# Performance work log

Hardware: AMD Instinct MI355X
Metric: run time of the kernel (lower is better)

## Reference

```python
import jax, jax.numpy as jnp
import numpy as np
from jax import lax

NEG = -1e30


def ctc_loss(log_probs, targets, input_lengths, target_lengths, blank=0):
    """CTC loss per sample (reduction='none').
    log_probs: [B,T,C] log-softmaxed. targets: [B,S] int (values != blank).
    Returns [B] negative log likelihoods.
    """
    B, T, C = log_probs.shape
    S = targets.shape[1]
    L = 2 * S + 1
    # extended label sequence with blanks interleaved: [b, t1, b, t2, ..., b]
    blanks = jnp.full((B, S), blank, targets.dtype)
    ext = jnp.concatenate(
        [jnp.stack([blanks, targets], axis=-1).reshape(B, 2 * S),
         jnp.full((B, 1), blank, targets.dtype)], axis=1)  # [B,L]
    # skip-transition allowed where ext[l] != blank and ext[l] != ext[l-2]
    prev2 = jnp.concatenate([jnp.full((B, 2), -1, ext.dtype), ext[:, :-2]], axis=1)
    allow_skip = (ext != blank) & (ext != prev2)  # [B,L]

    lp0 = jnp.take_along_axis(log_probs[:, 0, :], ext, axis=1)  # [B,L]
    alpha0 = jnp.where(jnp.arange(L)[None, :] < 2, lp0, NEG)

    def step(alpha, lp_t):  # lp_t: [B,C]
        lp = jnp.take_along_axis(lp_t, ext, axis=1)  # [B,L]
        a1 = alpha
        a2 = jnp.concatenate([jnp.full((B, 1), NEG), alpha[:, :-1]], axis=1)
        a3 = jnp.where(allow_skip,
                       jnp.concatenate([jnp.full((B, 2), NEG), alpha[:, :-2]], axis=1),
                       NEG)
        new = jax.nn.logsumexp(jnp.stack([a1, a2, a3]), axis=0) + lp
        return new, new

    _, alphas = lax.scan(step, alpha0, jnp.swapaxes(log_probs, 0, 1)[1:])
    alphas = jnp.concatenate([alpha0[None], alphas], axis=0)  # [T,B,L]

    t_idx = jnp.clip(input_lengths - 1, 0, T - 1)
    alpha_T = alphas[t_idx, jnp.arange(B)]  # [B,L]
    l1 = jnp.clip(2 * target_lengths, 0, L - 1)
    l2 = jnp.clip(2 * target_lengths - 1, 0, L - 1)
    last = jnp.take_along_axis(alpha_T, jnp.stack([l1, l2], axis=1), axis=1)  # [B,2]
    return -jax.nn.logsumexp(last, axis=1)


def focal_ctc(logits, targets, input_lengths, target_lengths, alpha=1.0, gamma=2.0):
    log_probs = jax.nn.log_softmax(logits, axis=-1)
    l = jnp.clip(ctc_loss(log_probs, targets, input_lengths, target_lengths), 1e-6, None)
    p_t = jnp.clip(jnp.exp(-l), 1e-6, 1.0)
    return jnp.mean(alpha * (1.0 - p_t) ** gamma * l)


def setup_inputs() -> dict:
    key = jax.random.key(0)
    ks = jax.random.split(key, 8)
    B, T = 32, 2000
    C_err, C_ph = 8, 128
    S_err, S_ph = 50, 200
    return {
        "error_logits": jax.random.normal(ks[0], (B, T, C_err), jnp.float32),
        "phoneme_logits": jax.random.normal(ks[1], (B, T, C_ph), jnp.float32),
        "error_targets": jax.random.randint(ks[2], (B, S_err), 1, C_err, jnp.int32),
        "phoneme_targets": jax.random.randint(ks[3], (B, S_ph), 1, C_ph, jnp.int32),
        "error_input_lengths": jnp.full((B,), T, jnp.int32),
        "phoneme_input_lengths": jnp.full((B,), T, jnp.int32),
        "error_target_lengths": jax.random.randint(ks[4], (B,), S_err // 2, S_err + 1, jnp.int32),
        "phoneme_target_lengths": jax.random.randint(ks[5], (B,), S_ph // 2, S_ph + 1, jnp.int32),
    }


def reference(error_logits, phoneme_logits, error_targets, phoneme_targets,
              error_input_lengths, phoneme_input_lengths,
              error_target_lengths, phoneme_target_lengths):
    error_weight, phoneme_weight = 1.0, 1.0
    err = focal_ctc(error_logits, error_targets, error_input_lengths, error_target_lengths)
    ph = focal_ctc(phoneme_logits, phoneme_targets, phoneme_input_lengths, phoneme_target_lengths)
    total = error_weight * err + phoneme_weight * ph
    return total, err, ph
```

## Files before the change

kernel.cpp:

```cpp
#include <hip/hip_runtime.h>
#include <hip/hip_bf16.h>

#define LOG2E 1.4426950408889634f
#define LN2   0.6931471805599453f
#define NEG2  (-1.4426950e30f)
#define EXP2F(x) __builtin_exp2f(x)
#define LOG2F(x) __builtin_log2f(x)
#define LDEXPF(x,k) __builtin_ldexpf((x),(k))

__device__ __forceinline__ float dpp_shr1_f(float x, float old) {
    return __int_as_float(__builtin_amdgcn_update_dpp(
        __float_as_int(old), __float_as_int(x), 0x138, 0xF, 0xF, false));
}
__device__ __forceinline__ int dpp_shr1_i(int x, int old) {
    return __builtin_amdgcn_update_dpp(old, x, 0x138, 0xF, 0xF, false);
}
__device__ __forceinline__ float dpp_shl1_f(float x, float old) {
    return __int_as_float(__builtin_amdgcn_update_dpp(
        __float_as_int(old), __float_as_int(x), 0x130, 0xF, 0xF, false));
}
__device__ __forceinline__ int dpp_shl1_i(int x, int old) {
    return __builtin_amdgcn_update_dpp(old, x, 0x130, 0xF, 0xF, false);
}

__device__ __forceinline__ unsigned bf16r(float x) {
    return (__float_as_uint(x) + 0x8000u) >> 16;
}

__device__ __forceinline__ void async16(void* lds, const void* g) {
    __builtin_amdgcn_global_load_lds(
        (const __attribute__((address_space(1))) unsigned int*)g,
        (__attribute__((address_space(3))) unsigned int*)lds, 16, 0, 0);
}
__device__ __forceinline__ void async4(void* lds, const void* g) {
    __builtin_amdgcn_global_load_lds(
        (const __attribute__((address_space(1))) unsigned int*)g,
        (__attribute__((address_space(3))) unsigned int*)lds, 4, 0, 0);
}

__device__ __forceinline__ void unpack8(const uint4& q, float (&p)[8]) {
    p[0] = __uint_as_float(q.x << 16);
    p[1] = __uint_as_float(q.x & 0xFFFF0000u);
    p[2] = __uint_as_float(q.y << 16);
    p[3] = __uint_as_float(q.y & 0xFFFF0000u);
    p[4] = __uint_as_float(q.z << 16);
    p[5] = __uint_as_float(q.z & 0xFFFF0000u);
    p[6] = __uint_as_float(q.w << 16);
    p[7] = __uint_as_float(q.w & 0xFFFF0000u);
}

__global__ __launch_bounds__(256) void prob_kernel(
    const float* __restrict__ ph_logits, const int* __restrict__ ph_tgt,
    unsigned short* __restrict__ Pph,
    const float* __restrict__ err_logits, const int* __restrict__ err_tgt,
    unsigned short* __restrict__ Perr) {
    int wid = threadIdx.x >> 6, lane = threadIdx.x & 63;
    __shared__ float ylds[4][128];
    if (blockIdx.x < 16000) {
        int r = blockIdx.x * 4 + wid;
        int b = r / 2000;
        const float* row = ph_logits + (size_t)r * 128;
        float y0 = row[lane] * LOG2E;
        float y1 = row[lane + 64] * LOG2E;
        ylds[wid][lane] = y0;
        ylds[wid][lane + 64] = y1;
        float m = fmaxf(y0, y1);
#pragma unroll
        for (int i = 1; i < 64; i <<= 1) m = fmaxf(m, __shfl_xor(m, i));
        float s = EXP2F(y0 - m) + EXP2F(y1 - m);
#pragma unroll
        for (int i = 1; i < 64; i <<= 1) s += __shfl_xor(s, i);
        float d2 = m + LOG2F(s);

        int c[4];
#pragma unroll
        for (int k = 0; k < 4; ++k) {
            int i = min(4 * lane + k, 199);
            c[k] = ph_tgt[b * 200 + i];
        }
        float pb = EXP2F(ylds[wid][0] - d2);
        float po[4];
#pragma unroll
        for (int k = 0; k < 4; ++k) po[k] = EXP2F(ylds[wid][c[k]] - d2);

        unsigned h[8];
#pragma unroll
        for (int s2 = 0; s2 < 8; ++s2) {
            int l = 8 * lane + s2;
            float v = (s2 & 1) ? po[s2 >> 1] : pb;
            h[s2] = (l <= 400) ? bf16r(v) : 0u;
        }
        uint4 u;
        u.x = h[0] | (h[1] << 16);
        u.y = h[2] | (h[3] << 16);
        u.z = h[4] | (h[5] << 16);
        u.w = h[6] | (h[7] << 16);
        *(uint4*)(Pph + (size_t)r * 512 + lane * 8) = u;
    } else {
        int r = (blockIdx.x - 16000) * 4 + wid;
        int b = r / 2000;
        const float* row = err_logits + (size_t)r * 8;
        float y = (lane < 8) ? row[lane] * LOG2E : -3.0e38f;
        if (lane < 8) ylds[wid][lane] = y;
        float m = y;
#pragma unroll
        for (int i = 1; i < 64; i <<= 1) m = fmaxf(m, __shfl_xor(m, i));
        float s = EXP2F(y - m);
#pragma unroll
        for (int i = 1; i < 64; i <<= 1) s += __shfl_xor(s, i);
        float d2 = m + LOG2F(s);

        int cc = err_tgt[b * 50 + min(lane, 49)];
        float pb = EXP2F(ylds[wid][0] - d2);
        float pod = EXP2F(ylds[wid][cc] - d2);
        int l0 = 2 * lane;
        unsigned h0 = (l0 <= 100) ? bf16r(pb) : 0u;
        unsigned h1 = (l0 + 1 <= 100) ? bf16r(pod) : 0u;
        *(unsigned*)(Perr + (size_t)r * 128 + lane * 2) = h0 | (h1 << 16);
    }
}

__device__ __forceinline__ void finish_loss(float capA, float capB, int capEA,
                                            int capEB, int lane,
                                            float* __restrict__ loss_out, int b) {
    float vA = (capA > 0.f) ? (float)capEA + LOG2F(capA) : NEG2;
    float vB = (capB > 0.f) ? (float)capEB + LOG2F(capB) : NEG2;
    float mm = fmaxf(vA, vB);
#pragma unroll
    for (int i = 1; i < 64; i <<= 1) mm = fmaxf(mm, __shfl_xor(mm, i));
    float sum = EXP2F(vA - mm) + EXP2F(vB - mm);
#pragma unroll
    for (int i = 1; i < 64; i <<= 1) sum += __shfl_xor(sum, i);
    if (lane == 0) loss_out[b] = -(mm + LOG2F(sum)) * LN2;
}

__global__ __launch_bounds__(64) void ctc7_kernel(
    const unsigned short* __restrict__ Perr, const unsigned short* __restrict__ Pph,
    const int* __restrict__ err_tgt, const int* __restrict__ ph_tgt,
    const int* __restrict__ err_il, const int* __restrict__ ph_il,
    const int* __restrict__ err_tl, const int* __restrict__ ph_tl,
    float* __restrict__ aerr, int* __restrict__ aerrE,
    float* __restrict__ gerr, int* __restrict__ gerrE,
    float* __restrict__ aph, int* __restrict__ aphE,
    float* __restrict__ gph, int* __restrict__ gphE,
    float* __restrict__ loss_err, float* __restrict__ loss_ph, int T) {
    __shared__ unsigned short ring[32 * 512];
    char* ringc = (char*)ring;
    const int blk = blockIdx.x;
    const int lane = threadIdx.x & 63;
    const int NR = T >> 1;
    const int NCH = NR >> 3;

    if (blk < 32) {
        const int b = blk;
        int t_idx = min(max(err_il[b] - 1, 0), T - 1);
        const int* tgt = err_tgt + b * 50;
        float skip1f;
        {
            int l = lane * 2 + 1; bool sk = false;
            if (l >= 3 && l <= 100) { int i = l >> 1; sk = (tgt[i] != tgt[i - 1]); }
            skip1f = sk ? 1.f : 0.f;
        }
        const char* base = (const char*)(Perr + (size_t)b * T * 128);
        float a0 = 0.f, a1 = 0.f; int E = 0; float f = 1.f;

        auto fstep = [&](unsigned cur) {
            float p0 = __uint_as_float(cur << 16);
            float p1 = __uint_as_float(cur & 0xFFFF0000u);
            float t1 = dpp_shr1_f(a1, 0.f) * f;
            float na0 = (a0 + t1) * p0;
            a1 = __builtin_fmaf(skip1f, t1, a1 + a0) * p1;
            a0 = na0;
        };
        auto rex = [&]() {
            float m = fmaxf(a0, a1);
            int k = ((__float_as_int(m) >> 23) & 255) - 127;
            a0 = LDEXPF(a0, -k); a1 = LDEXPF(a1, -k); E += k;
            int En = dpp_shr1_i(E, E);
            int Ep = max(E, En);
            int eo = E - Ep;
            a0 = LDEXPF(a0, eo); a1 = LDEXPF(a1, eo);
            E = Ep;
            int d = max(En - Ep, -127);
            f = __int_as_float((d + 127) << 23);
        };

        if (t_idx == T - 1) {
            const char* srcl = base + lane * 4;
            auto rd = [&](int row) -> unsigned {
                return *((const unsigned*)(ringc + (size_t)(row & 31) * 256) + lane);
            };
#pragma unroll
            for (int r = 0; r < 24; ++r)
                async4(ringc + (size_t)(r & 31) * 256, srcl + (size_t)r * 256);
            {
#pragma unroll
                for (int r = 24; r < 32; ++r)
                    async4(ringc + (size_t)(r & 31) * 256, srcl + (size_t)r * 256);
                asm volatile("s_waitcnt vmcnt(16)" ::: "memory");
                __builtin_amdgcn_sched_barrier(0);
                unsigned q[8];
#pragma unroll
                for (int j = 0; j < 8; ++j) q[j] = rd(j);
                float p0 = __uint_as_float(q[0] << 16);
                float p1 = __uint_as_float(q[0] & 0xFFFF0000u);
                a0 = (lane == 0) ? p0 : 0.f;
                a1 = (lane == 0) ? p1 : 0.f;
                E = 0; f = 1.f;
#pragma unroll
                for (int j = 1; j < 8; ++j) {
                    fstep(q[j]);
                    if (j == 3 || j == 7) rex();
                }
            }
            for (int k = 1; k < NCH; ++k) {
                if (k + 3 < NCH) {
                    int bs = (k + 3) * 8;
#pragma unroll
                    for (int r = 0; r < 8; ++r)
                        async4(ringc + (size_t)((bs + r) & 31) * 256,
                               srcl + (size_t)(bs + r) * 256);
                    asm volatile("s_waitcnt vmcnt(16)" ::: "memory");
                } else {
                    asm volatile("s_waitcnt vmcnt(0)" ::: "memory");
                }
                __builtin_amdgcn_sched_barrier(0);
                unsigned q[8];
#pragma unroll
                for (int j = 0; j < 8; ++j) q[j] = rd(k * 8 + j);
#pragma unroll
                for (int j = 0; j < 8; ++j) {
                    fstep(q[j]);
                    if (j == 3 || j == 7) rex();
                }
            }
            aerr[b * 128 + lane * 2] = a0;
            aerr[b * 128 + lane * 2 + 1] = a1;
            aerrE[b * 64 + lane] = E;
        } else {
            const int L = 101; int tl = err_tl[b];
            int l1 = min(2 * tl, L - 1), l2 = max(min(2 * tl - 1, L - 1), 0);
            float capA = 0.f, capB = 0.f; int capEA = 0, capEB = 0;
            for (int t = 0; t < T; ++t) {
                unsigned cur = *((const unsigned*)(base + (size_t)t * 256) + lane);
                float p0 = __uint_as_float(cur << 16);
                float p1 = __uint_as_float(cur & 0xFFFF0000u);
                if (t == 0) {
                    a0 = (lane == 0) ? p0 : 0.f;
                    a1 = (lane == 0) ? p1 : 0.f;
                    E = 0;
                } else {
                    float n1 = dpp_shr1_f(a1, 0.f);
                    int En = dpp_shr1_i(E, E);
                    int Ep = max(E, En);
                    float t1 = LDEXPF(n1, En - Ep);
                    float o0 = LDEXPF(a0, E - Ep), o1 = LDEXPF(a1, E - Ep);
                    E = Ep;
                    a0 = (o0 + t1) * p0;
                    a1 = __builtin_fmaf(skip1f, t1, o1 + o0) * p1;
                }
                if (t == t_idx) {
                    int l0 = lane * 2;
                    if (l0 == l1) { capA = a0; capEA = E; }
                    if (l0 == l2) { capB = a0; capEB = E; }
                    if (l0 + 1 == l1) { capA = a1; capEA = E; }
                    if (l0 + 1 == l2) { capB = a1; capEB = E; }
                }
                if ((t & 3) == 3) {
                    float m = fmaxf(a0, a1);
                    int k = ((__float_as_int(m) >> 23) & 255) - 127;
                    a0 = LDEXPF(a0, -k); a1 = LDEXPF(a1, -k); E += k;
                }
            }
            finish_loss(capA, capB, capEA, capEB, lane, loss_err, b);
        }

    } else if (blk < 64) {
        const int b = blk - 32;
        const int* tgt = err_tgt + b * 50;
        const int L = 101; int tl = err_tl[b];
        int l1 = min(2 * tl, L - 1), l2 = max(min(2 * tl - 1, L - 1), 0);
        float skip1f;
        {
            int l = lane * 2 + 1; bool sk = false;
            if (l >= 3 && l <= 100) { int i = l >> 1; sk = (tgt[i] != tgt[i - 1]); }
            skip1f = sk ? 1.f : 0.f;
        }
        float skp2 = dpp_shl1_f(skip1f, 0.f);
        const char* base = (const char*)(Perr + (size_t)b * T * 128);
        const char* srcl = base + (size_t)(T - 1) * 256 + lane * 4;
        auto rd = [&](int row) -> unsigned {
            return *((const unsigned*)(ringc + (size_t)(row & 31) * 256) + lane);
        };
        float g0 = 0.f, g1 = 0.f; int E = 0; float f = 1.f;
        auto bstep = [&](unsigned cur) {
            float p0 = __uint_as_float(cur << 16);
            float p1 = __uint_as_float(cur & 0xFFFF0000u);
            float t0 = dpp_shl1_f(g0, 0.f) * f;
            float t1 = dpp_shl1_f(g1, 0.f) * f;
            float ng0 = (g0 + g1) * p0;
            g1 = __builtin_fmaf(skp2, t1, g1 + t0) * p1;
            g0 = ng0;
        };
        auto rex = [&]() {
            float m = fmaxf(g0, g1);
            int k = ((__float_as_int(m) >> 23) & 255) - 127;
            g0 = LDEXPF(g0, -k); g1 = LDEXPF(g1, -k); E += k;
            int En = dpp_shl1_i(E, E);
            int Ep = max(E, En);
            int eo = E - Ep;
            g0 = LDEXPF(g0, eo); g1 = LDEXPF(g1, eo);
            E = Ep;
            int d = max(En - Ep, -127);
            f = __int_as_float((d + 127) << 23);
        };
#pragma unroll
        for (int r = 0; r < 24; ++r)
            async4(ringc + (size_t)(r & 31) * 256, srcl - (size_t)r * 256);
        {
#pragma unroll
            for (int r = 24; r < 32; ++r)
                async4(ringc + (size_t)(r & 31) * 256, srcl - (size_t)r * 256);
            asm volatile("s_waitcnt vmcnt(16)" ::: "memory");
            __builtin_amdgcn_sched_barrier(0);
            unsigned q[8];
#pragma unroll
            for (int j = 0; j < 8; ++j) q[j] = rd(j);
            float p0 = __uint_as_float(q[0] << 16);
            float p1 = __uint_as_float(q[0] & 0xFFFF0000u);
            int l0 = lane * 2;
            g0 = (l0 == l1 || l0 == l2) ? p0 : 0.f;
            g1 = (l0 + 1 == l1 || l0 + 1 == l2) ? p1 : 0.f;
            E = 0; f = 1.f;
#pragma unroll
            for (int j = 1; j < 8; ++j) {
                bstep(q[j]);
                if (j == 3 || j == 7) rex();
            }
        }
        for (int k = 1; k < NCH; ++k) {
            if (k + 3 < NCH) {
                int bs = (k + 3) * 8;
#pragma unroll
                for (int r = 0; r < 8; ++r)
                    async4(ringc + (size_t)((bs + r) & 31) * 256,
                           srcl - (size_t)(bs + r) * 256);
                asm volatile("s_waitcnt vmcnt(16)" ::: "memory");
            } else {
                asm volatile("s_waitcnt vmcnt(0)" ::: "memory");
            }
            __builtin_amdgcn_sched_barrier(0);
            unsigned q[8];
#pragma unroll
            for (int j = 0; j < 8; ++j) q[j] = rd(k * 8 + j);
#pragma unroll
            for (int j = 0; j < 8; ++j) {
                bstep(q[j]);
                if (j == 3 || j == 7) rex();
            }
        }
        gerr[b * 128 + lane * 2] = g0;
        gerr[b * 128 + lane * 2 + 1] = g1;
        gerrE[b * 64 + lane] = E;

    } else if (blk < 96) {
        const int b = blk - 64;
        int t_idx = min(max(ph_il[b] - 1, 0), T - 1);
        const int* tgt = ph_tgt + b * 200;
        float skf[8];
#pragma unroll
        for (int s = 0; s < 8; ++s) {
            int l = lane * 8 + s; float v = 0.f;
            if ((s & 1) && l >= 3 && l <= 400) {
                int i = l >> 1; v = (tgt[i] != tgt[i - 1]) ? 1.f : 0.f;
            }
            skf[s] = v;
        }
        const char* base = (const char*)(Pph + (size_t)b * T * 512);
        float a[8];
#pragma unroll
        for (int s = 0; s < 8; ++s) a[s] = 0.f;
        int E = 0; float f = 1.f;
        auto rd4 = [&](int row) -> uint4 {
            return *((const uint4*)(ringc + (size_t)(row & 31) * 1024) + lane);
        };
        auto fstep = [&](const uint4& q) {
            float p[8]; unpack8(q, p);
            float n7 = dpp_shr1_f(a[7], 0.f) * f;
            float n6 = dpp_shr1_f(a[6], 0.f) * f;
            float an[8];
#pragma unroll
            for (int s = 0; s < 8; ++s) {
                float am1 = (s == 0) ? n7 : a[s - 1];
                float am2 = (s == 0) ? n6 : ((s == 1) ? n7 : a[s - 2]);
                an[s] = __builtin_fmaf(skf[s], am2, a[s] + am1) * p[s];
            }
#pragma unroll
            for (int s = 0; s < 8; ++s) a[s] = an[s];
        };
        auto rex = [&]() {
            float m = a[0];
#pragma unroll
            for (int s = 1; s < 8; ++s) m = fmaxf(m, a[s]);
            int k = ((__float_as_int(m) >> 23) & 255) - 127;
#pragma unroll
            for (int s = 0; s < 8; ++s) a[s] = LDEXPF(a[s], -k);
            E += k;
            int En = dpp_shr1_i(E, E);
            int Ep = max(E, En);
            int eo = E - Ep;
#pragma unroll
            for (int s = 0; s < 8; ++s) a[s] = LDEXPF(a[s], eo);
            E = Ep;
            int d = max(En - Ep, -127);
            f = __int_as_float((d + 127) << 23);
        };

        if (t_idx == T - 1) {
            const char* srcl = base + lane * 16;
#pragma unroll
            for (int r = 0; r < 24; ++r)
                async16(ringc + (size_t)(r & 31) * 1024, srcl + (size_t)r * 1024);
            {
#pragma unroll
                for (int r = 24; r < 32; ++r)
                    async16(ringc + (size_t)(r & 31) * 1024, srcl + (size_t)r * 1024);
                asm volatile("s_waitcnt vmcnt(16)" ::: "memory");
                __builtin_amdgcn_sched_barrier(0);
                uint4 q[8];
#pragma unroll
                for (int j = 0; j < 8; ++j) q[j] = rd4(j);
                float p[8]; unpack8(q[0], p);
#pragma unroll
                for (int s = 0; s < 8; ++s) {
                    int l = lane * 8 + s;
                    a[s] = (l < 2) ? p[s] : 0.f;
                }
                E = 0; f = 1.f;
#pragma unroll
                for (int j = 1; j < 8; ++j) {
                    fstep(q[j]);
                    if (j == 3 || j == 7) rex();
                }
            }
            for (int k = 1; k < NCH; ++k) {
                if (k + 3 < NCH) {
                    int bs = (k + 3) * 8;
#pragma unroll
                    for (int r = 0; r < 8; ++r)
                        async16(ringc + (size_t)((bs + r) & 31) * 1024,
                                srcl + (size_t)(bs + r) * 1024);
                    asm volatile("s_waitcnt vmcnt(16)" ::: "memory");
                } else {
                    asm volatile("s_waitcnt vmcnt(0)" ::: "memory");
                }
                __builtin_amdgcn_sched_barrier(0);
                uint4 q[8];
#pragma unroll
                for (int j = 0; j < 8; ++j) q[j] = rd4(k * 8 + j);
#pragma unroll
                for (int j = 0; j < 8; ++j) {
                    fstep(q[j]);
                    if (j == 3 || j == 7) rex();
                }
            }
#pragma unroll
            for (int s = 0; s < 8; ++s) aph[b * 512 + lane * 8 + s] = a[s];
            aphE[b * 64 + lane] = E;
        } else {
            const int L = 401; int tl = ph_tl[b];
            int l1 = min(2 * tl, L - 1), l2 = max(min(2 * tl - 1, L - 1), 0);
            float capA = 0.f, capB = 0.f; int capEA = 0, capEB = 0;
            for (int t = 0; t < T; ++t) {
                uint4 q = *((const uint4*)(base + (size_t)t * 1024) + lane);
                float p[8]; unpack8(q, p);
                if (t == 0) {
#pragma unroll
                    for (int s = 0; s < 8; ++s) {
                        int l = lane * 8 + s;
                        a[s] = (l < 2) ? p[s] : 0.f;
                    }
                    E = 0;
                } else {
                    float n7 = dpp_shr1_f(a[7], 0.f), n6 = dpp_shr1_f(a[6], 0.f);
                    int En = dpp_shr1_i(E, E);
                    int Ep = max(E, En);
                    float o[8];
#pragma unroll
                    for (int s = 0; s < 8; ++s) o[s] = LDEXPF(a[s], E - Ep);
                    float s7 = LDEXPF(n7, En - Ep), s6 = LDEXPF(n6, En - Ep);
                    E = Ep;
#pragma unroll
                    for (int s = 0; s < 8; ++s) {
                        float am1 = (s == 0) ? s7 : o[s - 1];
                        float am2 = (s == 0) ? s6 : ((s == 1) ? s7 : o[s - 2]);
                        a[s] = __builtin_fmaf(skf[s], am2, o[s] + am1) * p[s];
                    }
                }
                if (t == t_idx) {
#pragma unroll
                    for (int s = 0; s < 8; ++s) {
                        int l = lane * 8 + s;
                        if (l == l1) { capA = a[s]; capEA = E; }
                        if (l == l2) { capB = a[s]; capEB = E; }
                    }
                }
                if ((t & 3) == 3) {
                    float m = a[0];
#pragma unroll
                    for (int s = 1; s < 8; ++s) m = fmaxf(m, a[s]);
                    int k = ((__float_as_int(m) >> 23) & 255) - 127;
#pragma unroll
                    for (int s = 0; s < 8; ++s) a[s] = LDEXPF(a[s], -k);
                    E += k;
                }
            }
            finish_loss(capA, capB, capEA, capEB, lane, loss_ph, b);
        }

    } else {
        const int b = blk - 96;
        const int* tgt = ph_tgt + b * 200;
        const int L = 401; int tl = ph_tl[b];
        int l1 = min(2 * tl, L - 1), l2 = max(min(2 * tl - 1, L - 1), 0);
        float skf[8];
#pragma unroll
        for (int s = 0; s < 8; ++s) {
            int l = lane * 8 + s; float v = 0.f;
            if ((s & 1) && l >= 3 && l <= 400) {
                int i = l >> 1; v = (tgt[i] != tgt[i - 1]) ? 1.f : 0.f;
            }
            skf[s] = v;
        }
        float nskf1 = dpp_shl1_f(skf[1], 0.f);
        float skp2[8];
        skp2[0] = 0.f; skp2[1] = skf[3]; skp2[2] = 0.f; skp2[3] = skf[5];
        skp2[4] = 0.f; skp2[5] = skf[7]; skp2[6] = 0.f; skp2[7] = nskf1;

        const char* base = (const char*)(Pph + (size_t)b * T * 512);
        const char* srcl = base + (size_t)(T - 1) * 1024 + lane * 16;
        auto rd4 = [&](int row) -> uint4 {
            return *((const uint4*)(ringc + (size_t)(row & 31) * 1024) + lane);
        };
        float g[8];
#pragma unroll
        for (int s = 0; s < 8; ++s) g[s] = 0.f;
        int E = 0; float f = 1.f;
        auto bstep = [&](const uint4& q) {
            float p[8]; unpack8(q, p);
            float nb0 = dpp_shl1_f(g[0], 0.f) * f;
            float nb1 = dpp_shl1_f(g[1], 0.f) * f;
            float gn[8];
#pragma unroll
            for (int s = 0; s < 8; ++s) {
                float bp1 = (s < 7) ? g[s + 1] : nb0;
                float bp2 = (s < 6) ? g[s + 2] : ((s == 6) ? nb0 : nb1);
                gn[s] = __builtin_fmaf(skp2[s], bp2, g[s] + bp1) * p[s];
            }
#pragma unroll
            for (int s = 0; s < 8; ++s) g[s] = gn[s];
        };
        auto rex = [&]() {
            float m = g[0];
#pragma unroll
            for (int s = 1; s < 8; ++s) m = fmaxf(m, g[s]);
            int k = ((__float_as_int(m) >> 23) & 255) - 127;
#pragma unroll
            for (int s = 0; s < 8; ++s) g[s] = LDEXPF(g[s], -k);
            E += k;
            int En = dpp_shl1_i(E, E);
            int Ep = max(E, En);
            int eo = E - Ep;
#pragma unroll
            for (int s = 0; s < 8; ++s) g[s] = LDEXPF(g[s], eo);
            E = Ep;
            int d = max(En - Ep, -127);
            f = __int_as_float((d + 127) << 23);
        };
#pragma unroll
        for (int r = 0; r < 24; ++r)
            async16(ringc + (size_t)(r & 31) * 1024, srcl - (size_t)r * 1024);
        {
#pragma unroll
            for (int r = 24; r < 32; ++r)
                async16(ringc + (size_t)(r & 31) * 1024, srcl - (size_t)r * 1024);
            asm volatile("s_waitcnt vmcnt(16)" ::: "memory");
            __builtin_amdgcn_sched_barrier(0);
            uint4 q[8];
#pragma unroll
            for (int j = 0; j < 8; ++j) q[j] = rd4(j);
            float p[8]; unpack8(q[0], p);
#pragma unroll
            for (int s = 0; s < 8; ++s) {
                int l = lane * 8 + s;
                g[s] = (l == l1 || l == l2) ? p[s] : 0.f;
            }
            E = 0; f = 1.f;
#pragma unroll
            for (int j = 1; j < 8; ++j) {
                bstep(q[j]);
                if (j == 3 || j == 7) rex();
            }
        }
        for (int k = 1; k < NCH; ++k) {
            if (k + 3 < NCH) {
                int bs = (k + 3) * 8;
#pragma unroll
                for (int r = 0; r < 8; ++r)
                    async16(ringc + (size_t)((bs + r) & 31) * 1024,
                            srcl - (size_t)(bs + r) * 1024);
                asm volatile("s_waitcnt vmcnt(16)" ::: "memory");
            } else {
                asm volatile("s_waitcnt vmcnt(0)" ::: "memory");
            }
            __builtin_amdgcn_sched_barrier(0);
            uint4 q[8];
#pragma unroll
            for (int j = 0; j < 8; ++j) q[j] = rd4(k * 8 + j);
#pragma unroll
            for (int j = 0; j < 8; ++j) {
                bstep(q[j]);
                if (j == 3 || j == 7) rex();
            }
        }
#pragma unroll
        for (int s = 0; s < 8; ++s) gph[b * 512 + lane * 8 + s] = g[s];
        gphE[b * 64 + lane] = E;
    }
}

__global__ __launch_bounds__(64) void combine_kernel(
    const int* __restrict__ err_tgt, const int* __restrict__ ph_tgt,
    const int* __restrict__ err_il, const int* __restrict__ ph_il,
    const float* __restrict__ aerr, const int* __restrict__ aerrE,
    const float* __restrict__ gerr, const int* __restrict__ gerrE,
    const float* __restrict__ aph, const int* __restrict__ aphE,
    const float* __restrict__ gph, const int* __restrict__ gphE,
    float* __restrict__ loss_err, float* __restrict__ loss_ph, int T) {
    const int blk = blockIdx.x;
    const int lane = threadIdx.x & 63;
    if (blk < 32) {
        const int b = blk;
        int t_idx = min(max(err_il[b] - 1, 0), T - 1);
        if (t_idx != T - 1) return;
        const int* tgt = err_tgt + b * 50;
        float skip1f;
        {
            int l = lane * 2 + 1; bool sk = false;
            if (l >= 3 && l <= 100) { int i = l >> 1; sk = (tgt[i] != tgt[i - 1]); }
            skip1f = sk ? 1.f : 0.f;
        }
        float a0 = aerr[b * 128 + lane * 2], a1 = aerr[b * 128 + lane * 2 + 1];
        int Ea = aerrE[b * 64 + lane];
        float g0 = gerr[b * 128 + lane * 2], g1 = gerr[b * 128 + lane * 2 + 1];
        int Eb = gerrE[b * 64 + lane];
        float nb0 = __shfl_down(g0, 1), nb1 = __shfl_down(g1, 1);
        int Ebn = __shfl_down(Eb, 1);
        float skp2 = __shfl_down(skip1f, 1);
        if (lane == 63) { nb0 = 0.f; nb1 = 0.f; Ebn = Eb; skp2 = 0.f; }
        int Em = max(Eb, Ebn);
        float o0 = LDEXPF(g0, Eb - Em), o1 = LDEXPF(g1, Eb - Em);
        float t0 = LDEXPF(nb0, Ebn - Em), t1 = LDEXPF(nb1, Ebn - Em);
        float bc0 = o0 + o1;
        float bc1 = __builtin_fmaf(skp2, t1, o1 + t0);
        float dot = __builtin_fmaf(a0, bc0, a1 * bc1);
        float v = (dot > 0.f) ? (float)(Ea + Em) + LOG2F(dot) : NEG2;
        float mm = v;
#pragma unroll
        for (int i = 1; i < 64; i <<= 1) mm = fmaxf(mm, __shfl_xor(mm, i));
        float sum = EXP2F(v - mm);
#pragma unroll
        for (int i = 1; i < 64; i <<= 1) sum += __shfl_xor(sum, i);
        if (lane == 0) loss_err[b] = -(mm + LOG2F(sum)) * LN2;
    } else {
        const int b = blk - 32;
        int t_idx = min(max(ph_il[b] - 1, 0), T - 1);
        if (t_idx != T - 1) return;
        const int* tgt = ph_tgt + b * 200;
        float skf[8];
#pragma unroll
        for (int s = 0; s < 8; ++s) {
            int l = lane * 8 + s; float v = 0.f;
            if ((s & 1) && l >= 3 && l <= 400) {
                int i = l >> 1; v = (tgt[i] != tgt[i - 1]) ? 1.f : 0.f;
            }
            skf[s] = v;
        }
        float a[8], g[8];
#pragma unroll
        for (int s = 0; s < 8; ++s) {
            a[s] = aph[b * 512 + lane * 8 + s];
            g[s] = gph[b * 512 + lane * 8 + s];
        }
        int Ea = aphE[b * 64 + lane];
        int Eb = gphE[b * 64 + lane];
        float nb0 = __shfl_down(g[0], 1), nb1 = __shfl_down(g[1], 1);
        int Ebn = __shfl_down(Eb, 1);
        float nskf1 = __shfl_down(skf[1], 1);
        if (lane == 63) { nb0 = 0.f; nb1 = 0.f; Ebn = Eb; nskf1 = 0.f; }
        float skp2[8];
        skp2[0] = 0.f; skp2[1] = skf[3]; skp2[2] = 0.f; skp2[3] = skf[5];
        skp2[4] = 0.f; skp2[5] = skf[7]; skp2[6] = 0.f; skp2[7] = nskf1;
        int Em = max(Eb, Ebn);
        float o[8];
#pragma unroll
        for (int s = 0; s < 8; ++s) o[s] = LDEXPF(g[s], Eb - Em);
        float t0 = LDEXPF(nb0, Ebn - Em), t1 = LDEXPF(nb1, Ebn - Em);
        float dot = 0.f;
#pragma unroll
        for (int s = 0; s < 8; ++s) {
            float bp1 = (s < 7) ? o[s + 1] : t0;
            float bp2 = (s < 6) ? o[s + 2] : ((s == 6) ? t0 : t1);
            float bc = __builtin_fmaf(skp2[s], bp2, o[s] + bp1);
            dot = __builtin_fmaf(a[s], bc, dot);
        }
        float v = (dot > 0.f) ? (float)(Ea + Em) + LOG2F(dot) : NEG2;
        float mm = v;
#pragma unroll
        for (int i = 1; i < 64; i <<= 1) mm = fmaxf(mm, __shfl_xor(mm, i));
        float sum = EXP2F(v - mm);
#pragma unroll
        for (int i = 1; i < 64; i <<= 1) sum += __shfl_xor(sum, i);
        if (lane == 0) loss_ph[b] = -(mm + LOG2F(sum)) * LN2;
    }
}

__global__ void denom_err_kernel(const float* __restrict__ logits,
                                 float* __restrict__ d2, int rows) {
    int r = blockIdx.x * blockDim.x + threadIdx.x;
    if (r >= rows) return;
    const float* row = logits + (size_t)r * 8;
    float x[8];
#pragma unroll
    for (int i = 0; i < 8; ++i) x[i] = row[i] * LOG2E;
    float m = x[0];
#pragma unroll
    for (int i = 1; i < 8; ++i) m = fmaxf(m, x[i]);
    float s = 0.f;
#pragma unroll
    for (int i = 0; i < 8; ++i) s += EXP2F(x[i] - m);
    d2[r] = m + LOG2F(s);
}

__global__ void denom_ph_kernel(const float* __restrict__ logits,
                                float* __restrict__ d2, int rows) {
    int wave = (int)((blockIdx.x * (size_t)blockDim.x + threadIdx.x) >> 6);
    int lane = threadIdx.x & 63;
    if (wave >= rows) return;
    const float* row = logits + (size_t)wave * 128;
    float x0 = row[lane] * LOG2E;
    float x1 = row[lane + 64] * LOG2E;
    float m = fmaxf(x0, x1);
#pragma unroll
    for (int i = 1; i < 64; i <<= 1) m = fmaxf(m, __shfl_xor(m, i));
    float s = EXP2F(x0 - m) + EXP2F(x1 - m);
#pragma unroll
    for (int i = 1; i < 64; i <<= 1) s += __shfl_xor(s, i);
    if (lane == 0) d2[wave] = m + LOG2F(s);
}

template <int NST, int C>
__device__ __forceinline__ void gather_row(const float* ringL, const float* ringD,
                                           int row, const int (&clsoff)[NST],
                                           float (&g)[NST], float& gd) {
    int base = (row & 63) * C;
#pragma unroll
    for (int s = 0; s < NST; ++s) g[s] = ringL[base + clsoff[s]];
    gd = ringD[row & 63];
}

template <int C, int CHV>
__device__ __forceinline__ void stage_load(const float* __restrict__ lrow,
                                           const float* __restrict__ d2row,
                                           int t0, int T, int lane,
                                           float4 (&st)[CHV], float4& stD) {
#pragma unroll
    for (int j = 0; j < CHV; ++j) {
        int e = t0 * C + (j * 64 + lane) * 4;
        e = min(e, T * C - 4);
        st[j] = *(const float4*)(lrow + e);
    }
    if (lane < 8) {
        int e = t0 + lane * 4;
        e = min(e, T - 4);
        stD = *(const float4*)(d2row + e);
    }
}

template <int C, int CHV>
__device__ __forceinline__ void stage_write(float* ringL, float* ringD, int t0, int lane,
                                            const float4 (&st)[CHV], const float4& stD) {
    int base = (t0 & 63) * C;
#pragma unroll
    for (int j = 0; j < CHV; ++j)
        *(float4*)(ringL + base + (j * 64 + lane) * 4) = st[j];
    if (lane < 8)
        *(float4*)(ringD + (t0 & 63) + lane * 4) = stD;
}

template <int NST>
__device__ __forceinline__ void do_step_lin(
    float (&a)[NST], int& E,
    const float (&g)[NST], float gd,
    const float (&validf)[NST], const bool (&skipb)[NST],
    int lane, int t, int t_idx, int l1, int l2,
    float& capA, float& capB, int& capEA, int& capEB) {
    float p[NST];
#pragma unroll
    for (int s = 0; s < NST; ++s)
        p[s] = validf[s] * EXP2F(__builtin_fmaf(g[s], LOG2E, -gd));
    if (t == 0) {
#pragma unroll
        for (int s = 0; s < NST; ++s) {
            int l = lane * NST + s;
            a[s] = (l < 2) ? p[s] : 0.f;
        }
        E = 0;
    } else {
        float top1 = dpp_shr1_f(a[NST - 1], 0.f);
        int   En   = dpp_shr1_i(E, E);
        int Ep = max(E, En);
        float t1 = LDEXPF(top1, En - Ep);
        float ao[NST];
#pragma unroll
        for (int s = 0; s < NST; ++s) ao[s] = LDEXPF(a[s], E - Ep);
        E = Ep;
#pragma unroll
        for (int s = 0; s < NST; ++s) {
            float sum;
            if (s == 0)            sum = ao[0] + t1;
            else if (s == 1)       sum = ao[1] + ao[0] + (skipb[1] ? t1 : 0.f);
            else if ((s & 1) == 0) sum = ao[s] + ao[s - 1];
            else                   sum = ao[s] + ao[s - 1] + (skipb[s] ? ao[s - 2] : 0.f);
            a[s] = sum * p[s];
        }
    }
    if (t == t_idx) {
#pragma unroll
        for (int s = 0; s < NST; ++s) {
            int l = lane * NST + s;
            if (l == l1) { capA = a[s]; capEA = E; }
            if (l == l2) { capB = a[s]; capEB = E; }
        }
    }
    if ((t & 1) == 1) {
        float m = a[0];
#pragma unroll
        for (int s = 1; s < NST; ++s) m = fmaxf(m, a[s]);
        int k = ((__float_as_int(m) >> 23) & 255) - 127;
#pragma unroll
        for (int s = 0; s < NST; ++s) a[s] = LDEXPF(a[s], -k);
        E += k;
    }
}

template <int NST, int C, int S, int CHV>
__device__ __forceinline__ void ctc_run(
    const float* __restrict__ lrow, const float* __restrict__ d2row,
    const int* __restrict__ tgt, int T, int t_idx, int l1, int l2,
    float* ringL, float* ringD, float* __restrict__ loss_out, int b) {
    const int lane = threadIdx.x & 63;
    const int L = 2 * S + 1;
    int clsoff[NST];
    bool skipb[NST];
    float validf[NST];
#pragma unroll
    for (int s = 0; s < NST; ++s) {
        int l = lane * NST + s;
        bool v = (l < L);
        int li = v ? l : 0;
        int c = 0;
        bool sk = false;
        if (li & 1) {
            int i = li >> 1;
            c = tgt[i];
            if (li >= 3) sk = (c != tgt[i - 1]);
        }
        clsoff[s] = c;
        skipb[s] = sk;
        validf[s] = v ? 1.f : 0.f;
    }
    float4 st[CHV];
    float4 stD = make_float4(0.f, 0.f, 0.f, 0.f);
    stage_load<C, CHV>(lrow, d2row, 0, T, lane, st, stD);
    stage_write<C, CHV>(ringL, ringD, 0, lane, st, stD);
    stage_load<C, CHV>(lrow, d2row, 32, T, lane, st, stD);
    stage_write<C, CHV>(ringL, ringD, 32, lane, st, stD);
    stage_load<C, CHV>(lrow, d2row, 64, T, lane, st, stD);
    float gA[NST], gB[NST], dA, dB;
    gather_row<NST, C>(ringL, ringD, 0, clsoff, gA, dA);
    gather_row<NST, C>(ringL, ringD, 1, clsoff, gB, dB);
    float a[NST];
#pragma unroll
    for (int s = 0; s < NST; ++s) a[s] = 0.f;
    int E = 0;
    float capA = 0.f, capB = 0.f;
    int capEA = 0, capEB = 0;
    const int NCH = (T + 31) >> 5;
    for (int c = 0; c < NCH; ++c) {
        int t0 = c << 5;
        int half = min(32, T - t0) >> 1;
        for (int j = 0; j < half; ++j) {
            int t = t0 + 2 * j;
            do_step_lin<NST>(a, E, gA, dA, validf, skipb, lane, t, t_idx, l1, l2,
                             capA, capB, capEA, capEB);
            gather_row<NST, C>(ringL, ringD, t + 2, clsoff, gA, dA);
            do_step_lin<NST>(a, E, gB, dB, validf, skipb, lane, t + 1, t_idx, l1, l2,
                             capA, capB, capEA, capEB);
            gather_row<NST, C>(ringL, ringD, t + 3, clsoff, gB, dB);
            if (j == 14 && c + 2 < NCH) {
                stage_write<C, CHV>(ringL, ringD, t0 + 64, lane, st, stD);
                if (c + 3 < NCH)
                    stage_load<C, CHV>(lrow, d2row, t0 + 96, T, lane, st, stD);
            }
        }
    }
    float vA = (capA > 0.f) ? (float)capEA + LOG2F(capA) : NEG2;
    float vB = (capB > 0.f) ? (float)capEB + LOG2F(capB) : NEG2;
    float mm = fmaxf(vA, vB);
#pragma unroll
    for (int i = 1; i < 64; i <<= 1) mm = fmaxf(mm, __shfl_xor(mm, i));
    float sum = EXP2F(vA - mm) + EXP2F(vB - mm);
#pragma unroll
    for (int i = 1; i < 64; i <<= 1) sum += __shfl_xor(sum, i);
    if (lane == 0) loss_out[b] = -(mm + LOG2F(sum)) * LN2;
}

__global__ __launch_bounds__(64) void ctc_kernel(
    const float* __restrict__ err_logits, const float* __restrict__ ph_logits,
    const int* __restrict__ err_tgt, const int* __restrict__ ph_tgt,
    const int* __restrict__ err_il, const int* __restrict__ ph_il,
    const int* __restrict__ err_tl, const int* __restrict__ ph_tl,
    const float* __restrict__ d2_err, const float* __restrict__ d2_ph,
    float* __restrict__ loss_err, float* __restrict__ loss_ph, int T) {
    __shared__ float ringL[64 * 128];
    __shared__ float ringD[64];
    int blk = blockIdx.x;
    if (blk < 32) {
        int b = blk;
        const int L = 101;
        int tl = err_tl[b];
        int l1 = min(2 * tl, L - 1);
        int l2 = max(min(2 * tl - 1, L - 1), 0);
        int t_idx = min(max(err_il[b] - 1, 0), T - 1);
        ctc_run<2, 8, 50, 1>(err_logits + (size_t)b * T * 8, d2_err + (size_t)b * T,
                             err_tgt + b * 50, T, t_idx, l1, l2, ringL, ringD,
                             loss_err, b);
    } else {
        int b = blk - 32;
        const int L = 401;
        int tl = ph_tl[b];
        int l1 = min(2 * tl, L - 1);
        int l2 = max(min(2 * tl - 1, L - 1), 0);
        int t_idx = min(max(ph_il[b] - 1, 0), T - 1);
        ctc_run<8, 128, 200, 16>(ph_logits + (size_t)b * T * 128, d2_ph + (size_t)b * T,
                                 ph_tgt + b * 200, T, t_idx, l1, l2, ringL, ringD,
                                 loss_ph, b);
    }
}

__global__ void final_kernel(const float* __restrict__ loss_err,
                             const float* __restrict__ loss_ph,
                             float* __restrict__ out) {
    int lane = threadIdx.x & 63;
    float fe = 0.f, fp = 0.f;
    if (lane < 32) {
        float l = fmaxf(loss_err[lane], 1e-6f);
        float pt = fminf(fmaxf(EXP2F(-l * LOG2E), 1e-6f), 1.0f);
        float om = 1.f - pt;
        fe = om * om * l;
        l = fmaxf(loss_ph[lane], 1e-6f);
        pt = fminf(fmaxf(EXP2F(-l * LOG2E), 1e-6f), 1.0f);
        om = 1.f - pt;
        fp = om * om * l;
    }
#pragma unroll
    for (int i = 1; i < 64; i <<= 1) {
        fe += __shfl_xor(fe, i);
        fp += __shfl_xor(fp, i);
    }
    if (lane == 0) {
        float err = fe / 32.f;
        float ph = fp / 32.f;
        out[0] = err + ph;
        out[1] = err;
        out[2] = ph;
    }
}

extern "C" void kernel_launch(void* const* d_in, const int* in_sizes, int n_in,
                              void* d_out, int out_size, void* d_ws, size_t ws_size,
                              hipStream_t stream) {
    const int B = 32, T = 2000;
    const float* err_logits = (const float*)d_in[0];
    const float* ph_logits  = (const float*)d_in[1];
    const int* err_tgt = (const int*)d_in[2];
    const int* ph_tgt  = (const int*)d_in[3];
    const int* err_il  = (const int*)d_in[4];
    const int* ph_il   = (const int*)d_in[5];
    const int* err_tl  = (const int*)d_in[6];
    const int* ph_tl   = (const int*)d_in[7];
    float* out = (float*)d_out;

    const size_t PH_US  = (size_t)B * T * 512;
    const size_t ERR_US = (size_t)B * T * 128;

    char* p = (char*)d_ws;
    unsigned short* Pph  = (unsigned short*)p; p += PH_US * 2;
    unsigned short* Perr = (unsigned short*)p; p += ERR_US * 2;
    float* aph  = (float*)p; p += (size_t)B * 512 * 4;
    int*   aphE = (int*)p;   p += (size_t)B * 64 * 4;
    float* gph  = (float*)p; p += (size_t)B * 512 * 4;
    int*   gphE = (int*)p;   p += (size_t)B * 64 * 4;
    float* aerr = (float*)p; p += (size_t)B * 128 * 4;
    int*   aerrE= (int*)p;   p += (size_t)B * 64 * 4;
    float* gerr = (float*)p; p += (size_t)B * 128 * 4;
    int*   gerrE= (int*)p;   p += (size_t)B * 64 * 4;
    float* loss_err = (float*)p; p += B * 4;
    float* loss_ph  = (float*)p; p += B * 4;
    const size_t need = (size_t)(p - (char*)d_ws);

    if (ws_size >= need) {
        prob_kernel<<<32000, 256, 0, stream>>>(ph_logits, ph_tgt, Pph,
                                               err_logits, err_tgt, Perr);
        ctc7_kernel<<<128, 64, 0, stream>>>(Perr, Pph, err_tgt, ph_tgt,
                                            err_il, ph_il, err_tl, ph_tl,
                                            aerr, aerrE, gerr, gerrE,
                                            aph, aphE, gph, gphE,
                                            loss_err, loss_ph, T);
        combine_kernel<<<64, 64, 0, stream>>>(err_tgt, ph_tgt, err_il, ph_il,
                                              aerr, aerrE, gerr, gerrE,
                                              aph, aphE, gph, gphE,
                                              loss_err, loss_ph, T);
        final_kernel<<<1, 64, 0, stream>>>(loss_err, loss_ph, out);
    } else {
        float* ws = (float*)d_ws;
        float* d2_err   = ws;
        float* d2_ph    = ws + 64000;
        float* le = ws + 128000;
        float* lp = ws + 128032;
        int rows = B * T;
        denom_err_kernel<<<(rows + 255) / 256, 256, 0, stream>>>(err_logits, d2_err, rows);
        denom_ph_kernel<<<rows / 4, 256, 0, stream>>>(ph_logits, d2_ph, rows);
        ctc_kernel<<<64, 64, 0, stream>>>(err_logits, ph_logits, err_tgt, ph_tgt,
                                          err_il, ph_il, err_tl, ph_tl,
                                          d2_err, d2_ph, le, lp, T);
        final_kernel<<<1, 64, 0, stream>>>(le, lp, out);
    }
}
```

Before: 167.8 us.

## Store phoneme probabilities as fp32 when workspace allows, streamline CTC recurrence

New measurement: 172.0 us. +2.5%, slower.

```diff
diff --git a/kernel.cpp b/kernel.cpp
--- a/kernel.cpp
+++ b/kernel.cpp
@@ -49,9 +49,10 @@
     p[7] = __uint_as_float(q.w & 0xFFFF0000u);
 }
 
+template <bool PHF32>
 __global__ __launch_bounds__(256) void prob_kernel(
     const float* __restrict__ ph_logits, const int* __restrict__ ph_tgt,
-    unsigned short* __restrict__ Pph,
+    void* __restrict__ Pph_,
     const float* __restrict__ err_logits, const int* __restrict__ err_tgt,
     unsigned short* __restrict__ Perr) {
     int wid = threadIdx.x >> 6, lane = threadIdx.x & 63;
@@ -83,19 +84,32 @@
 #pragma unroll
         for (int k = 0; k < 4; ++k) po[k] = EXP2F(ylds[wid][c[k]] - d2);
 
-        unsigned h[8];
+        float vv[8];
 #pragma unroll
         for (int s2 = 0; s2 < 8; ++s2) {
             int l = 8 * lane + s2;
             float v = (s2 & 1) ? po[s2 >> 1] : pb;
-            h[s2] = (l <= 400) ? bf16r(v) : 0u;
-        }
-        uint4 u;
-        u.x = h[0] | (h[1] << 16);
-        u.y = h[2] | (h[3] << 16);
-        u.z = h[4] | (h[5] << 16);
-        u.w = h[6] | (h[7] << 16);
-        *(uint4*)(Pph + (size_t)r * 512 + lane * 8) = u;
+            vv[s2] = (l <= 400) ? v : 0.f;
+        }
+        if constexpr (PHF32) {
+            float* P = (float*)Pph_;
+            *(float4*)(P + (size_t)r * 512 + lane * 8) =
+                make_float4(vv[0], vv[1], vv[2], vv[3]);
+            *(float4*)(P + (size_t)r * 512 + lane * 8 + 4) =
+                make_float4(vv[4], vv[5], vv[6], vv[7]);
+        } else {
+            unsigned short* P = (unsigned short*)Pph_;
+            unsigned h[8];
+#pragma unroll
+            for (int s2 = 0; s2 < 8; ++s2)
+                h[s2] = (vv[s2] > 0.f || ((8 * lane + s2) <= 400)) ? bf16r(vv[s2]) : 0u;
+            uint4 u;
+            u.x = h[0] | (h[1] << 16);
+            u.y = h[2] | (h[3] << 16);
+            u.z = h[4] | (h[5] << 16);
+            u.w = h[6] | (h[7] << 16);
+            *(uint4*)(P + (size_t)r * 512 + lane * 8) = u;
+        }
     } else {
         int r = (blockIdx.x - 16000) * 4 + wid;
         int b = r / 2000;
@@ -134,8 +148,9 @@
     if (lane == 0) loss_out[b] = -(mm + LOG2F(sum)) * LN2;
 }
 
-__global__ __launch_bounds__(64) void ctc7_kernel(
-    const unsigned short* __restrict__ Perr, const unsigned short* __restrict__ Pph,
+template <bool PHF32>
+__global__ __launch_bounds__(64) void ctc8_kernel(
+    const unsigned short* __restrict__ Perr, const void* __restrict__ Pph_,
     const int* __restrict__ err_tgt, const int* __restrict__ ph_tgt,
     const int* __restrict__ err_il, const int* __restrict__ ph_il,
     const int* __restrict__ err_tl, const int* __restrict__ ph_tl,
@@ -144,8 +159,9 @@
     float* __restrict__ aph, int* __restrict__ aphE,
     float* __restrict__ gph, int* __restrict__ gphE,
     float* __restrict__ loss_err, float* __restrict__ loss_ph, int T) {
-    __shared__ unsigned short ring[32 * 512];
-    char* ringc = (char*)ring;
+    constexpr int RB = PHF32 ? 2048 : 1024;
+    __shared__ unsigned char ring_[32 * RB];
+    char* ringc = (char*)ring_;
     const int blk = blockIdx.x;
     const int lane = threadIdx.x & 63;
     const int NR = T >> 1;
@@ -175,11 +191,11 @@
         auto rex = [&]() {
             float m = fmaxf(a0, a1);
             int k = ((__float_as_int(m) >> 23) & 255) - 127;
-            a0 = LDEXPF(a0, -k); a1 = LDEXPF(a1, -k); E += k;
-            int En = dpp_shr1_i(E, E);
-            int Ep = max(E, En);
-            int eo = E - Ep;
-            a0 = LDEXPF(a0, eo); a1 = LDEXPF(a1, eo);
+            int E2 = E + k;
+            int En = dpp_shr1_i(E2, E2);
+            int Ep = max(E2, En);
+            int sc = (E2 - Ep) - k;
+            a0 = LDEXPF(a0, sc); a1 = LDEXPF(a1, sc);
             E = Ep;
             int d = max(En - Ep, -127);
             f = __int_as_float((d + 127) << 23);
@@ -210,7 +226,7 @@
 #pragma unroll
                 for (int j = 1; j < 8; ++j) {
                     fstep(q[j]);
-                    if (j == 3 || j == 7) rex();
+                    if (j == 7) rex();
                 }
             }
             for (int k = 1; k < NCH; ++k) {
@@ -231,7 +247,7 @@
 #pragma unroll
                 for (int j = 0; j < 8; ++j) {
                     fstep(q[j]);
-                    if (j == 3 || j == 7) rex();
+                    if (j == 7) rex();
                 }
             }
             aerr[b * 128 + lane * 2] = a0;
@@ -305,11 +321,11 @@
         auto rex = [&]() {
             float m = fmaxf(g0, g1);
             int k = ((__float_as_int(m) >> 23) & 255) - 127;
-            g0 = LDEXPF(g0, -k); g1 = LDEXPF(g1, -k); E += k;
-            int En = dpp_shl1_i(E, E);
-            int Ep = max(E, En);
-            int eo = E - Ep;
-            g0 = LDEXPF(g0, eo); g1 = LDEXPF(g1, eo);
+            int E2 = E + k;
+            int En = dpp_shl1_i(E2, E2);
+            int Ep = max(E2, En);
+            int sc = (E2 - Ep) - k;
+            g0 = LDEXPF(g0, sc); g1 = LDEXPF(g1, sc);
             E = Ep;
             int d = max(En - Ep, -127);
             f = __int_as_float((d + 127) << 23);
@@ -335,7 +351,7 @@
 #pragma unroll
             for (int j = 1; j < 8; ++j) {
                 bstep(q[j]);
-                if (j == 3 || j == 7) rex();
+                if (j == 7) rex();
             }
         }
         for (int k = 1; k < NCH; ++k) {
@@ -356,7 +372,7 @@
 #pragma unroll
             for (int j = 0; j < 8; ++j) {
                 bstep(q[j]);
-                if (j == 3 || j == 7) rex();
+                if (j == 7) rex();
             }
         }
         gerr[b * 128 + lane * 2] = g0;
@@ -376,92 +392,104 @@
             }
             skf[s] = v;
         }
-        const char* base = (const char*)(Pph + (size_t)b * T * 512);
+        const char* baseP = (const char*)Pph_ + (size_t)b * T * RB;
         float a[8];
 #pragma unroll
         for (int s = 0; s < 8; ++s) a[s] = 0.f;
         int E = 0; float f = 1.f;
-        auto rd4 = [&](int row) -> uint4 {
-            return *((const uint4*)(ringc + (size_t)(row & 31) * 1024) + lane);
-        };
-        auto fstep = [&](const uint4& q) {
-            float p[8]; unpack8(q, p);
+
+        auto rdrow = [&](int row, float (&p)[8]) {
+            const char* ra = ringc + (size_t)(row & 31) * RB;
+            if constexpr (PHF32) {
+                float4 qa = *(const float4*)(ra + lane * 32);
+                float4 qb = *(const float4*)(ra + lane * 32 + 16);
+                p[0] = qa.x; p[1] = qa.y; p[2] = qa.z; p[3] = qa.w;
+                p[4] = qb.x; p[5] = qb.y; p[6] = qb.z; p[7] = qb.w;
+            } else {
+                uint4 q = *((const uint4*)ra + lane);
+                unpack8(q, p);
+            }
+        };
+        auto fstep = [&](const float (&p)[8]) {
             float n7 = dpp_shr1_f(a[7], 0.f) * f;
             float n6 = dpp_shr1_f(a[6], 0.f) * f;
-            float an[8];
-#pragma unroll
-            for (int s = 0; s < 8; ++s) {
-                float am1 = (s == 0) ? n7 : a[s - 1];
-                float am2 = (s == 0) ? n6 : ((s == 1) ? n7 : a[s - 2]);
-                an[s] = __builtin_fmaf(skf[s], am2, a[s] + am1) * p[s];
-            }
-#pragma unroll
-            for (int s = 0; s < 8; ++s) a[s] = an[s];
+            float an0 = (a[0] + n7) * p[0];
+            float an1 = __builtin_fmaf(skf[1], n7, a[1] + a[0]) * p[1];
+            float an2 = (a[2] + a[1]) * p[2];
+            float an3 = __builtin_fmaf(skf[3], a[1], a[3] + a[2]) * p[3];
+            float an4 = (a[4] + a[3]) * p[4];
+            float an5 = __builtin_fmaf(skf[5], a[3], a[5] + a[4]) * p[5];
+            float an6 = (a[6] + a[5]) * p[6];
+            float an7 = __builtin_fmaf(skf[7], a[5], a[7] + a[6]) * p[7];
+            a[0] = an0; a[1] = an1; a[2] = an2; a[3] = an3;
+            a[4] = an4; a[5] = an5; a[6] = an6; a[7] = an7;
         };
         auto rex = [&]() {
             float m = a[0];
 #pragma unroll
             for (int s = 1; s < 8; ++s) m = fmaxf(m, a[s]);
             int k = ((__float_as_int(m) >> 23) & 255) - 127;
-#pragma unroll
-            for (int s = 0; s < 8; ++s) a[s] = LDEXPF(a[s], -k);
-            E += k;
-            int En = dpp_shr1_i(E, E);
-            int Ep = max(E, En);
-            int eo = E - Ep;
-#pragma unroll
-            for (int s = 0; s < 8; ++s) a[s] = LDEXPF(a[s], eo);
+            int E2 = E + k;
+            int En = dpp_shr1_i(E2, E2);
+            int Ep = max(E2, En);
+            int sc = (E2 - Ep) - k;
+#pragma unroll
+            for (int s = 0; s < 8; ++s) a[s] = LDEXPF(a[s], sc);
             E = Ep;
             int d = max(En - Ep, -127);
             f = __int_as_float((d + 127) << 23);
         };
+        auto issue_row = [&](int r) {
+            char* d = ringc + (size_t)(r & 31) * RB;
+            const char* s0 = baseP + (size_t)r * RB + lane * 16;
+            async16(d, s0);
+            if constexpr (PHF32) async16(d + 1024, s0 + 1024);
+        };
+        auto vwait = [&]() {
+            if constexpr (PHF32) asm volatile("s_waitcnt vmcnt(32)" ::: "memory");
+            else                 asm volatile("s_waitcnt vmcnt(16)" ::: "memory");
+        };
 
         if (t_idx == T - 1) {
-            const char* srcl = base + lane * 16;
-#pragma unroll
-            for (int r = 0; r < 24; ++r)
-                async16(ringc + (size_t)(r & 31) * 1024, srcl + (size_t)r * 1024);
+            float pA[8], pB[8];
+#pragma unroll
+            for (int r = 0; r < 24; ++r) issue_row(r);
             {
 #pragma unroll
-                for (int r = 24; r < 32; ++r)
-                    async16(ringc + (size_t)(r & 31) * 1024, srcl + (size_t)r * 1024);
-                asm volatile("s_waitcnt vmcnt(16)" ::: "memory");
+                for (int r = 24; r < 32; ++r) issue_row(r);
+                vwait();
                 __builtin_amdgcn_sched_barrier(0);
-                uint4 q[8];
-#pragma unroll
-                for (int j = 0; j < 8; ++j) q[j] = rd4(j);
-                float p[8]; unpack8(q[0], p);
+                rdrow(0, pA); rdrow(1, pB);
 #pragma unroll
                 for (int s = 0; s < 8; ++s) {
                     int l = lane * 8 + s;
-                    a[s] = (l < 2) ? p[s] : 0.f;
+                    a[s] = (l < 2) ? pA[s] : 0.f;
                 }
                 E = 0; f = 1.f;
+                rdrow(2, pA);
 #pragma unroll
                 for (int j = 1; j < 8; ++j) {
-                    fstep(q[j]);
-                    if (j == 3 || j == 7) rex();
+                    if (j & 1) { fstep(pB); rdrow(j + 2, pB); }
+                    else       { fstep(pA); rdrow(j + 2, pA); }
+                    if (j == 7) rex();
                 }
             }
             for (int k = 1; k < NCH; ++k) {
                 if (k + 3 < NCH) {
                     int bs = (k + 3) * 8;
 #pragma unroll
-                    for (int r = 0; r < 8; ++r)
-                        async16(ringc + (size_t)((bs + r) & 31) * 1024,
-                                srcl + (size_t)(bs + r) * 1024);
-                    asm volatile("s_waitcnt vmcnt(16)" ::: "memory");
+                    for (int r = 0; r < 8; ++r) issue_row(bs + r);
+                    vwait();
                 } else {
                     asm volatile("s_waitcnt vmcnt(0)" ::: "memory");
                 }
                 __builtin_amdgcn_sched_barrier(0);
-                uint4 q[8];
-#pragma unroll
-                for (int j = 0; j < 8; ++j) q[j] = rd4(k * 8 + j);
 #pragma unroll
                 for (int j = 0; j < 8; ++j) {
-                    fstep(q[j]);
-                    if (j == 3 || j == 7) rex();
+                    int t = k * 8 + j;
+                    if (t & 1) { fstep(pB); rdrow(t + 2, pB); }
+                    else       { fstep(pA); rdrow(t + 2, pA); }
+                    if (j == 7) rex();
                 }
             }
 #pragma unroll
@@ -472,8 +500,16 @@
             int l1 = min(2 * tl, L - 1), l2 = max(min(2 * tl - 1, L - 1), 0);
             float capA = 0.f, capB = 0.f; int capEA = 0, capEB = 0;
             for (int t = 0; t < T; ++t) {
-                uint4 q = *((const uint4*)(base + (size_t)t * 1024) + lane);
-                float p[8]; unpack8(q, p);
+                float p[8];
+                if constexpr (PHF32) {
+                    const float4* rp = (const float4*)(baseP + (size_t)t * RB);
+                    float4 qa = rp[lane * 2], qb = rp[lane * 2 + 1];
+                    p[0] = qa.x; p[1] = qa.y; p[2] = qa.z; p[3] = qa.w;
+                    p[4] = qb.x; p[5] = qb.y; p[6] = qb.z; p[7] = qb.w;
+                } else {
+                    uint4 q = *((const uint4*)(baseP + (size_t)t * RB) + lane);
+                    unpack8(q, p);
+                }
                 if (t == 0) {
 #pragma unroll
                     for (int s = 0; s < 8; ++s) {
@@ -533,94 +569,106 @@
             skf[s] = v;
         }
         float nskf1 = dpp_shl1_f(skf[1], 0.f);
-        float skp2[8];
-        skp2[0] = 0.f; skp2[1] = skf[3]; skp2[2] = 0.f; skp2[3] = skf[5];
-        skp2[4] = 0.f; skp2[5] = skf[7]; skp2[6] = 0.f; skp2[7] = nskf1;
-
-        const char* base = (const char*)(Pph + (size_t)b * T * 512);
-        const char* srcl = base + (size_t)(T - 1) * 1024 + lane * 16;
-        auto rd4 = [&](int row) -> uint4 {
-            return *((const uint4*)(ringc + (size_t)(row & 31) * 1024) + lane);
-        };
+        float sk1 = skf[3], sk3 = skf[5], sk5 = skf[7], sk7 = nskf1;
+
+        const char* baseP = (const char*)Pph_ + (size_t)b * T * RB;
+        const char* srcTop = baseP + (size_t)(T - 1) * RB + lane * 16;
         float g[8];
 #pragma unroll
         for (int s = 0; s < 8; ++s) g[s] = 0.f;
         int E = 0; float f = 1.f;
-        auto bstep = [&](const uint4& q) {
-            float p[8]; unpack8(q, p);
+
+        auto rdrow = [&](int row, float (&p)[8]) {
+            const char* ra = ringc + (size_t)(row & 31) * RB;
+            if constexpr (PHF32) {
+                float4 qa = *(const float4*)(ra + lane * 32);
+                float4 qb = *(const float4*)(ra + lane * 32 + 16);
+                p[0] = qa.x; p[1] = qa.y; p[2] = qa.z; p[3] = qa.w;
+                p[4] = qb.x; p[5] = qb.y; p[6] = qb.z; p[7] = qb.w;
+            } else {
+                uint4 q = *((const uint4*)ra + lane);
+                unpack8(q, p);
+            }
+        };
+        auto bstep = [&](const float (&p)[8]) {
             float nb0 = dpp_shl1_f(g[0], 0.f) * f;
             float nb1 = dpp_shl1_f(g[1], 0.f) * f;
-            float gn[8];
-#pragma unroll
-            for (int s = 0; s < 8; ++s) {
-                float bp1 = (s < 7) ? g[s + 1] : nb0;
-                float bp2 = (s < 6) ? g[s + 2] : ((s == 6) ? nb0 : nb1);
-                gn[s] = __builtin_fmaf(skp2[s], bp2, g[s] + bp1) * p[s];
-            }
-#pragma unroll
-            for (int s = 0; s < 8; ++s) g[s] = gn[s];
+            float gn0 = (g[0] + g[1]) * p[0];
+            float gn1 = __builtin_fmaf(sk1, g[3], g[1] + g[2]) * p[1];
+            float gn2 = (g[2] + g[3]) * p[2];
+            float gn3 = __builtin_fmaf(sk3, g[5], g[3] + g[4]) * p[3];
+            float gn4 = (g[4] + g[5]) * p[4];
+            float gn5 = __builtin_fmaf(sk5, g[7], g[5] + g[6]) * p[5];
+            float gn6 = (g[6] + g[7]) * p[6];
+            float gn7 = __builtin_fmaf(sk7, nb1, g[7] + nb0) * p[7];
+            g[0] = gn0; g[1] = gn1; g[2] = gn2; g[3] = gn3;
+            g[4] = gn4; g[5] = gn5; g[6] = gn6; g[7] = gn7;
         };
         auto rex = [&]() {
             float m = g[0];
 #pragma unroll
             for (int s = 1; s < 8; ++s) m = fmaxf(m, g[s]);
             int k = ((__float_as_int(m) >> 23) & 255) - 127;
-#pragma unroll
-            for (int s = 0; s < 8; ++s) g[s] = LDEXPF(g[s], -k);
-            E += k;
-            int En = dpp_shl1_i(E, E);
-            int Ep = max(E, En);
-            int eo = E - Ep;
-#pragma unroll
-            for (int s = 0; s < 8; ++s) g[s] = LDEXPF(g[s], eo);
+            int E2 = E + k;
+            int En = dpp_shl1_i(E2, E2);
+            int Ep = max(E2, En);
+            int sc = (E2 - Ep) - k;
+#pragma unroll
+            for (int s = 0; s < 8; ++s) g[s] = LDEXPF(g[s], sc);
             E = Ep;
             int d = max(En - Ep, -127);
             f = __int_as_float((d + 127) << 23);
         };
-#pragma unroll
-        for (int r = 0; r < 24; ++r)
-            async16(ringc + (size_t)(r & 31) * 1024, srcl - (size_t)r * 1024);
+        auto issue_row = [&](int r) {
+            char* d = ringc + (size_t)(r & 31) * RB;
+            const char* s0 = srcTop - (size_t)r * RB;
+            async16(d, s0);
+            if constexpr (PHF32) async16(d + 1024, s0 + 1024);
+        };
+        auto vwait = [&]() {
+            if constexpr (PHF32) asm volatile("s_waitcnt vmcnt(32)" ::: "memory");
+            else                 asm volatile("s_waitcnt vmcnt(16)" ::: "memory");
+        };
+
+        float pA[8], pB[8];
+#pragma unroll
+        for (int r = 0; r < 24; ++r) issue_row(r);
         {
 #pragma unroll
-            for (int r = 24; r < 32; ++r)
-                async16(ringc + (size_t)(r & 31) * 1024, srcl - (size_t)r * 1024);
-            asm volatile("s_waitcnt vmcnt(16)" ::: "memory");
+            for (int r = 24; r < 32; ++r) issue_row(r);
+            vwait();
             __builtin_amdgcn_sched_barrier(0);
-            uint4 q[8];
-#pragma unroll
-            for (int j = 0; j < 8; ++j) q[j] = rd4(j);
-            float p[8]; unpack8(q[0], p);
+            rdrow(0, pA); rdrow(1, pB);
 #pragma unroll
             for (int s = 0; s < 8; ++s) {
                 int l = lane * 8 + s;
-                g[s] = (l == l1 || l == l2) ? p[s] : 0.f;
+                g[s] = (l == l1 || l == l2) ? pA[s] : 0.f;
             }
             E = 0; f = 1.f;
+            rdrow(2, pA);
 #pragma unroll
             for (int j = 1; j < 8; ++j) {
-                bstep(q[j]);
-                if (j == 3 || j == 7) rex();
+                if (j & 1) { bstep(pB); rdrow(j + 2, pB); }
+                else       { bstep(pA); rdrow(j + 2, pA); }
+                if (j == 7) rex();
             }
         }
         for (int k = 1; k < NCH; ++k) {
             if (k + 3 < NCH) {
                 int bs = (k + 3) * 8;
 #pragma unroll
-                for (int r = 0; r < 8; ++r)
-                    async16(ringc + (size_t)((bs + r) & 31) * 1024,
-                            srcl - (size_t)(bs + r) * 1024);
-                asm volatile("s_waitcnt vmcnt(16)" ::: "memory");
+                for (int r = 0; r < 8; ++r) issue_row(bs + r);
+                vwait();
             } else {
                 asm volatile("s_waitcnt vmcnt(0)" ::: "memory");
             }
             __builtin_amdgcn_sched_barrier(0);
-            uint4 q[8];
-#pragma unroll
-            for (int j = 0; j < 8; ++j) q[j] = rd4(k * 8 + j);
 #pragma unroll
             for (int j = 0; j < 8; ++j) {
-                bstep(q[j]);
-                if (j == 3 || j == 7) rex();
+                int t = k * 8 + j;
+                if (t & 1) { bstep(pB); rdrow(t + 2, pB); }
+                else       { bstep(pA); rdrow(t + 2, pA); }
+                if (j == 7) rex();
             }
         }
 #pragma unroll
@@ -725,240 +773,6 @@
     }
 }
 
-__global__ void denom_err_kernel(const float* __restrict__ logits,
-                                 float* __restrict__ d2, int rows) {
-    int r = blockIdx.x * blockDim.x + threadIdx.x;
-    if (r >= rows) return;
-    const float* row = logits + (size_t)r * 8;
-    float x[8];
-#pragma unroll
-    for (int i = 0; i < 8; ++i) x[i] = row[i] * LOG2E;
-    float m = x[0];
-#pragma unroll
-    for (int i = 1; i < 8; ++i) m = fmaxf(m, x[i]);
-    float s = 0.f;
-#pragma unroll
-    for (int i = 0; i < 8; ++i) s += EXP2F(x[i] - m);
-    d2[r] = m + LOG2F(s);
-}
-
-__global__ void denom_ph_kernel(const float* __restrict__ logits,
-                                float* __restrict__ d2, int rows) {
-    int wave = (int)((blockIdx.x * (size_t)blockDim.x + threadIdx.x) >> 6);
-    int lane = threadIdx.x & 63;
-    if (wave >= rows) return;
-    const float* row = logits + (size_t)wave * 128;
-    float x0 = row[lane] * LOG2E;
-    float x1 = row[lane + 64] * LOG2E;
-    float m = fmaxf(x0, x1);
-#pragma unroll
-    for (int i = 1; i < 64; i <<= 1) m = fmaxf(m, __shfl_xor(m, i));
-    float s = EXP2F(x0 - m) + EXP2F(x1 - m);
-#pragma unroll
-    for (int i = 1; i < 64; i <<= 1) s += __shfl_xor(s, i);
-    if (lane == 0) d2[wave] = m + LOG2F(s);
-}
-
-template <int NST, int C>
-__device__ __forceinline__ void gather_row(const float* ringL, const float* ringD,
-                                           int row, const int (&clsoff)[NST],
-                                           float (&g)[NST], float& gd) {
-    int base = (row & 63) * C;
-#pragma unroll
-    for (int s = 0; s < NST; ++s) g[s] = ringL[base + clsoff[s]];
-    gd = ringD[row & 63];
-}
-
-template <int C, int CHV>
-__device__ __forceinline__ void stage_load(const float* __restrict__ lrow,
-                                           const float* __restrict__ d2row,
-                                           int t0, int T, int lane,
-                                           float4 (&st)[CHV], float4& stD) {
-#pragma unroll
-    for (int j = 0; j < CHV; ++j) {
-        int e = t0 * C + (j * 64 + lane) * 4;
-        e = min(e, T * C - 4);
-        st[j] = *(const float4*)(lrow + e);
-    }
-    if (lane < 8) {
-        int e = t0 + lane * 4;
-        e = min(e, T - 4);
-        stD = *(const float4*)(d2row + e);
-    }
-}
-
-template <int C, int CHV>
-__device__ __forceinline__ void stage_write(float* ringL, float* ringD, int t0, int lane,
-                                            const float4 (&st)[CHV], const float4& stD) {
-    int base = (t0 & 63) * C;
-#pragma unroll
-    for (int j = 0; j < CHV; ++j)
-        *(float4*)(ringL + base + (j * 64 + lane) * 4) = st[j];
-    if (lane < 8)
-        *(float4*)(ringD + (t0 & 63) + lane * 4) = stD;
-}
-
-template <int NST>
-__device__ __forceinline__ void do_step_lin(
-    float (&a)[NST], int& E,
-    const float (&g)[NST], float gd,
-    const float (&validf)[NST], const bool (&skipb)[NST],
-    int lane, int t, int t_idx, int l1, int l2,
-    float& capA, float& capB, int& capEA, int& capEB) {
-    float p[NST];
-#pragma unroll
-    for (int s = 0; s < NST; ++s)
-        p[s] = validf[s] * EXP2F(__builtin_fmaf(g[s], LOG2E, -gd));
-    if (t == 0) {
-#pragma unroll
-        for (int s = 0; s < NST; ++s) {
-            int l = lane * NST + s;
-            a[s] = (l < 2) ? p[s] : 0.f;
-        }
-        E = 0;
-    } else {
-        float top1 = dpp_shr1_f(a[NST - 1], 0.f);
-        int   En   = dpp_shr1_i(E, E);
-        int Ep = max(E, En);
-        float t1 = LDEXPF(top1, En - Ep);
-        float ao[NST];
-#pragma unroll
-        for (int s = 0; s < NST; ++s) ao[s] = LDEXPF(a[s], E - Ep);
-        E = Ep;
-#pragma unroll
-        for (int s = 0; s < NST; ++s) {
-            float sum;
-            if (s == 0)            sum = ao[0] + t1;
-            else if (s == 1)       sum = ao[1] + ao[0] + (skipb[1] ? t1 : 0.f);
-            else if ((s & 1) == 0) sum = ao[s] + ao[s - 1];
-            else                   sum = ao[s] + ao[s - 1] + (skipb[s] ? ao[s - 2] : 0.f);
-            a[s] = sum * p[s];
-        }
-    }
-    if (t == t_idx) {
-#pragma unroll
-        for (int s = 0; s < NST; ++s) {
-            int l = lane * NST + s;
-            if (l == l1) { capA = a[s]; capEA = E; }
-            if (l == l2) { capB = a[s]; capEB = E; }
-        }
-    }
-    if ((t & 1) == 1) {
-        float m = a[0];
-#pragma unroll
-        for (int s = 1; s < NST; ++s) m = fmaxf(m, a[s]);
-        int k = ((__float_as_int(m) >> 23) & 255) - 127;
-#pragma unroll
-        for (int s = 0; s < NST; ++s) a[s] = LDEXPF(a[s], -k);
-        E += k;
-    }
-}
-
-template <int NST, int C, int S, int CHV>
-__device__ __forceinline__ void ctc_run(
-    const float* __restrict__ lrow, const float* __restrict__ d2row,
-    const int* __restrict__ tgt, int T, int t_idx, int l1, int l2,
-    float* ringL, float* ringD, float* __restrict__ loss_out, int b) {
-    const int lane = threadIdx.x & 63;
-    const int L = 2 * S + 1;
-    int clsoff[NST];
-    bool skipb[NST];
-    float validf[NST];
-#pragma unroll
-    for (int s = 0; s < NST; ++s) {
-        int l = lane * NST + s;
-        bool v = (l < L);
-        int li = v ? l : 0;
-        int c = 0;
-        bool sk = false;
-        if (li & 1) {
-            int i = li >> 1;
-            c = tgt[i];
-            if (li >= 3) sk = (c != tgt[i - 1]);
-        }
-        clsoff[s] = c;
-        skipb[s] = sk;
-        validf[s] = v ? 1.f : 0.f;
-    }
-    float4 st[CHV];
-    float4 stD = make_float4(0.f, 0.f, 0.f, 0.f);
-    stage_load<C, CHV>(lrow, d2row, 0, T, lane, st, stD);
-    stage_write<C, CHV>(ringL, ringD, 0, lane, st, stD);
-    stage_load<C, CHV>(lrow, d2row, 32, T, lane, st, stD);
-    stage_write<C, CHV>(ringL, ringD, 32, lane, st, stD);
-    stage_load<C, CHV>(lrow, d2row, 64, T, lane, st, stD);
-    float gA[NST], gB[NST], dA, dB;
-    gather_row<NST, C>(ringL, ringD, 0, clsoff, gA, dA);
-    gather_row<NST, C>(ringL, ringD, 1, clsoff, gB, dB);
-    float a[NST];
-#pragma unroll
-    for (int s = 0; s < NST; ++s) a[s] = 0.f;
-    int E = 0;
-    float capA = 0.f, capB = 0.f;
-    int capEA = 0, capEB = 0;
-    const int NCH = (T + 31) >> 5;
-    for (int c = 0; c < NCH; ++c) {
-        int t0 = c << 5;
-        int half = min(32, T - t0) >> 1;
-        for (int j = 0; j < half; ++j) {
-            int t = t0 + 2 * j;
-            do_step_lin<NST>(a, E, gA, dA, validf, skipb, lane, t, t_idx, l1, l2,
-                             capA, capB, capEA, capEB);
-            gather_row<NST, C>(ringL, ringD, t + 2, clsoff, gA, dA);
-            do_step_lin<NST>(a, E, gB, dB, validf, skipb, lane, t + 1, t_idx, l1, l2,
-                             capA, capB, capEA, capEB);
-            gather_row<NST, C>(ringL, ringD, t + 3, clsoff, gB, dB);
-            if (j == 14 && c + 2 < NCH) {
-                stage_write<C, CHV>(ringL, ringD, t0 + 64, lane, st, stD);
-                if (c + 3 < NCH)
-                    stage_load<C, CHV>(lrow, d2row, t0 + 96, T, lane, st, stD);
-            }
-        }
-    }
-    float vA = (capA > 0.f) ? (float)capEA + LOG2F(capA) : NEG2;
-    float vB = (capB > 0.f) ? (float)capEB + LOG2F(capB) : NEG2;
-    float mm = fmaxf(vA, vB);
-#pragma unroll
-    for (int i = 1; i < 64; i <<= 1) mm = fmaxf(mm, __shfl_xor(mm, i));
-    float sum = EXP2F(vA - mm) + EXP2F(vB - mm);
-#pragma unroll
-    for (int i = 1; i < 64; i <<= 1) sum += __shfl_xor(sum, i);
-    if (lane == 0) loss_out[b] = -(mm + LOG2F(sum)) * LN2;
-}
-
-__global__ __launch_bounds__(64) void ctc_kernel(
-    const float* __restrict__ err_logits, const float* __restrict__ ph_logits,
-    const int* __restrict__ err_tgt, const int* __restrict__ ph_tgt,
-    const int* __restrict__ err_il, const int* __restrict__ ph_il,
-    const int* __restrict__ err_tl, const int* __restrict__ ph_tl,
-    const float* __restrict__ d2_err, const float* __restrict__ d2_ph,
-    float* __restrict__ loss_err, float* __restrict__ loss_ph, int T) {
-    __shared__ float ringL[64 * 128];
-    __shared__ float ringD[64];
-    int blk = blockIdx.x;
-    if (blk < 32) {
-        int b = blk;
-        const int L = 101;
-        int tl = err_tl[b];
-        int l1 = min(2 * tl, L - 1);
-        int l2 = max(min(2 * tl - 1, L - 1), 0);
-        int t_idx = min(max(err_il[b] - 1, 0), T - 1);
-        ctc_run<2, 8, 50, 1>(err_logits + (size_t)b * T * 8, d2_err + (size_t)b * T,
-                             err_tgt + b * 50, T, t_idx, l1, l2, ringL, ringD,
-                             loss_err, b);
-    } else {
-        int b = blk - 32;
-        const int L = 401;
-        int tl = ph_tl[b];
-        int l1 = min(2 * tl, L - 1);
-        int l2 = max(min(2 * tl - 1, L - 1), 0);
-        int t_idx = min(max(ph_il[b] - 1, 0), T - 1);
-        ctc_run<8, 128, 200, 16>(ph_logits + (size_t)b * T * 128, d2_ph + (size_t)b * T,
-                                 ph_tgt + b * 200, T, t_idx, l1, l2, ringL, ringD,
-                                 loss_ph, b);
-    }
-}
-
 __global__ void final_kernel(const float* __restrict__ loss_err,
                              const float* __restrict__ loss_ph,
                              float* __restrict__ out) {
@@ -1002,12 +816,18 @@
     const int* ph_tl   = (const int*)d_in[7];
     float* out = (float*)d_out;
 
-    const size_t PH_US  = (size_t)B * T * 512;
-    const size_t ERR_US = (size_t)B * T * 128;
+    const size_t PH_F32_B  = (size_t)B * T * 512 * 4;
+    const size_t PH_BF16_B = (size_t)B * T * 512 * 2;
+    const size_t ERR_B     = (size_t)B * T * 128 * 2;
+    const size_t STATE_B   = ((size_t)B * 512 * 4) * 2 + ((size_t)B * 64 * 4) * 4 +
+                             ((size_t)B * 128 * 4) * 2 + (size_t)B * 4 * 2 + 1024;
+
+    const bool f32ok = ws_size >= PH_F32_B + ERR_B + STATE_B;
+    const size_t phB = f32ok ? PH_F32_B : PH_BF16_B;
 
     char* p = (char*)d_ws;
-    unsigned short* Pph  = (unsigned short*)p; p += PH_US * 2;
-    unsigned short* Perr = (unsigned short*)p; p += ERR_US * 2;
+    void* Pph = (void*)p;                 p += phB;
+    unsigned short* Perr = (unsigned short*)p; p += ERR_B;
     float* aph  = (float*)p; p += (size_t)B * 512 * 4;
     int*   aphE = (int*)p;   p += (size_t)B * 64 * 4;
     float* gph  = (float*)p; p += (size_t)B * 512 * 4;
@@ -1018,33 +838,27 @@
     int*   gerrE= (int*)p;   p += (size_t)B * 64 * 4;
     float* loss_err = (float*)p; p += B * 4;
     float* loss_ph  = (float*)p; p += B * 4;
-    const size_t need = (size_t)(p - (char*)d_ws);
-
-    if (ws_size >= need) {
-        prob_kernel<<<32000, 256, 0, stream>>>(ph_logits, ph_tgt, Pph,
-                                               err_logits, err_tgt, Perr);
-        ctc7_kernel<<<128, 64, 0, stream>>>(Perr, Pph, err_tgt, ph_tgt,
-                                            err_il, ph_il, err_tl, ph_tl,
-                                            aerr, aerrE, gerr, gerrE,
-                                            aph, aphE, gph, gphE,
-                                            loss_err, loss_ph, T);
-        combine_kernel<<<64, 64, 0, stream>>>(err_tgt, ph_tgt, err_il, ph_il,
-                                              aerr, aerrE, gerr, gerrE,
-                                              aph, aphE, gph, gphE,
-                                              loss_err, loss_ph, T);
-        final_kernel<<<1, 64, 0, stream>>>(loss_err, loss_ph, out);
+
+    if (f32ok) {
+        prob_kernel<true><<<32000, 256, 0, stream>>>(ph_logits, ph_tgt, Pph,
+                                                     err_logits, err_tgt, Perr);
+        ctc8_kernel<true><<<128, 64, 0, stream>>>(Perr, Pph, err_tgt, ph_tgt,
+                                                  err_il, ph_il, err_tl, ph_tl,
+                                                  aerr, aerrE, gerr, gerrE,
+                                                  aph, aphE, gph, gphE,
+                                                  loss_err, loss_ph, T);
     } else {
-        float* ws = (float*)d_ws;
-        float* d2_err   = ws;
-        float* d2_ph    = ws + 64000;
-        float* le = ws + 128000;
-        float* lp = ws + 128032;
-        int rows = B * T;
-        denom_err_kernel<<<(rows + 255) / 256, 256, 0, stream>>>(err_logits, d2_err, rows);
-        denom_ph_kernel<<<rows / 4, 256, 0, stream>>>(ph_logits, d2_ph, rows);
-        ctc_kernel<<<64, 64, 0, stream>>>(err_logits, ph_logits, err_tgt, ph_tgt,
-                                          err_il, ph_il, err_tl, ph_tl,
-                                          d2_err, d2_ph, le, lp, T);
-        final_kernel<<<1, 64, 0, stream>>>(le, lp, out);
+        prob_kernel<false><<<32000, 256, 0, stream>>>(ph_logits, ph_tgt, Pph,
+                                                      err_logits, err_tgt, Perr);
+        ctc8_kernel<false><<<128, 64, 0, stream>>>(Perr, Pph, err_tgt, ph_tgt,
+                                                   err_il, ph_il, err_tl, ph_tl,
+                                                   aerr, aerrE, gerr, gerrE,
+                                                   aph, aphE, gph, gphE,
+                                                   loss_err, loss_ph, T);
     }
-}
+    combine_kernel<<<64, 64, 0, stream>>>(err_tgt, ph_tgt, err_il, ph_il,
+                                          aerr, aerrE, gerr, gerrE,
+                                          aph, aphE, gph, gphE,
+                                          loss_err, loss_ph, T);
+    final_kernel<<<1, 64, 0, stream>>>(loss_err, loss_ph, out);
+}
```
